# Optimization experiments

Hardware: AMD Instinct MI355X
Metric: run time of the kernel (lower is better)

The kernel has to match this reference:

```python
import jax, jax.numpy as jnp
import numpy as np
import math

# init config (matches init_kwargs); sigma/alpha are squared in __init__
SIGMA2 = 8.0 ** 2
ALPHA2 = 8.0 ** 2
C_SIZE = 512
STRIDE = 8
MINX = 1e-06
M = 100                      # ratio=100 > 1 -> M = int(ratio), capped at 100
K = C_SIZE // STRIDE         # 64 grid cells per axis
G = K * K                    # 4096 density-field cells
B, N = 8, 512                # images, annotated points per image
TWO_PI = 2.0 * math.pi


def setup_inputs():
    key = jax.random.key(0)
    k1, _ = jax.random.split(key)
    points = jax.random.uniform(k1, (B, N, 2), dtype=jnp.float32) * C_SIZE
    st_sizes = jnp.full((B,), float(C_SIZE), dtype=jnp.float32)
    return {"points": points, "st_sizes": st_sizes}


def _per_image(pts, cood):
    # pts: [N,2]; cood: [K]
    x = pts[:, 0]
    y = pts[:, 1]
    dx = x[:, None] - cood[None, :]                 # [N,K]
    dy = y[:, None] - cood[None, :]                 # [N,K]
    # dis_all = y_dis[:, :, None] + x_dis[:, None, :] flattened: g = iy*K + ix
    dis = (dy[:, :, None] ** 2 + dx[:, None, :] ** 2).reshape(pts.shape[0], G)  # [N,G]
    s1 = ALPHA2 + SIGMA2
    s2 = ALPHA2 + SIGMA2 / 2.0
    m = jnp.exp(-0.5 / s1 * dis) / (TWO_PI * s1)    # [N,G]
    tv = jnp.exp(-0.5 / s2 * dis) / (TWO_PI * s2)
    v = (tv / (TWO_PI * 2.0 * SIGMA2)).sum(0) - (m ** 2).sum(0)   # [G] (sel_v == v, no bg)
    # top-M cells by sel_v, then sort indices ascending (ratio>1 branch -> static M)
    inds = jnp.argsort(-v)
    Minds = jnp.sort(inds[:M])                      # [M]
    v = jnp.maximum(v, MINX)                        # add=False -> clamp
    # xf[n, iy*K+ix] = x_n - cood[ix]; yf[n, iy*K+ix] = y_n - cood[iy]
    iy = Minds // K
    ix = Minds % K
    xfM = dx[:, ix]                                 # [N,M]
    yfM = dy[:, iy]                                 # [N,M]
    df = (xfM[:, None, :] - xfM[:, :, None]) ** 2 + (yfM[:, None, :] - yfM[:, :, None]) ** 2
    af = (0.5 * (xfM[:, None, :] + xfM[:, :, None])) ** 2 + (0.5 * (yfM[:, None, :] + yfM[:, :, None])) ** 2
    g1 = jnp.exp(-0.5 / (2.0 * SIGMA2) * df) / (TWO_PI * 2.0 * SIGMA2)          # [N,M,M]
    tmpv2 = (g1 * (jnp.exp(-0.5 / s2 * af) / (TWO_PI * s2))).sum(0) + g1.sum(0)  # [M,M]
    disM = dis[:, Minds]                            # [N,M]
    tmpm2 = jnp.exp(-0.5 / s1 * disM) / (TWO_PI * s1)
    A = tmpv2 - tmpm2.T @ tmpm2                     # [M,M]
    eye = jnp.eye(M, dtype=bool)
    A = jnp.where(eye, 1e-10, A)                    # diag overwritten to 1e-10
    vM = v[Minds] + 1e-10
    tmpA = vM[:, None] * jnp.linalg.inv(A) * vM[None, :] + jnp.diag(vM)
    Bm = jnp.linalg.inv(tmpA)
    return m, v, A, Bm, Minds


def reference(points, st_sizes):
    # st_sizes only matters for use_background=True; kept for signature fidelity
    cood = jnp.arange(0, C_SIZE, STRIDE, dtype=jnp.float32) + STRIDE / 2.0
    m, v, A, Bm, Minds = jax.vmap(lambda p: _per_image(p, cood))(points)
    return m, v, A, Bm, Minds
```

## Files before the change

### kernel.cpp

```cpp
#include <hip/hip_runtime.h>
#include <math.h>

#ifndef M_PI
#define M_PI 3.14159265358979323846
#endif

#define BB 8
#define NN 512
#define KK 64
#define GG 4096
#define MM 100

#define SZ_VD    (BB*GG*8u)
#define OFF_VD   0u
#define SZ_VM    (BB*MM*8u)
#define OFF_VM   (OFF_VD + SZ_VD)
#define SZ_AD    (BB*MM*MM*8u)
#define OFF_AD   (OFF_VM + SZ_VM)
#define OFF_MIND (OFF_AD + SZ_AD)

#define OUT_M  0
#define OUT_V  (BB*NN*GG)
#define OUT_A  (OUT_V + BB*GG)
#define OUT_B  (OUT_A + BB*MM*MM)
#define OUT_MI (OUT_B + BB*MM*MM)

#define MU_VP 4096
#define MU_AS 2048
#define MU_IV 10240

__device__ __forceinline__ void m_one_unit(const float* __restrict__ pts,
                                           float* __restrict__ out, int u) {
  int t = u*256 + (int)threadIdx.x;
  int e = t << 2;
  int img = e >> 21;
  int rem = e & ((1 << 21) - 1);
  int n = rem >> 12;
  int g = rem & 4095;
  int iy = g >> 6, ix = g & 63;
  const float CM = (float)(1.0/(2.0*M_PI*128.0));
  float x = pts[(img*NN + n)*2 + 0];
  float y = pts[(img*NN + n)*2 + 1];
  float dy = y - (8.0f*iy + 4.0f);
  float ey = __expf(dy*dy*(-0.5f/128.0f));
  float4 r;
  float dx0 = x - (8.0f*ix + 4.0f);
  float dx1 = x - (8.0f*(ix+1) + 4.0f);
  float dx2 = x - (8.0f*(ix+2) + 4.0f);
  float dx3 = x - (8.0f*(ix+3) + 4.0f);
  r.x = ey*__expf(dx0*dx0*(-0.5f/128.0f))*CM;
  r.y = ey*__expf(dx1*dx1*(-0.5f/128.0f))*CM;
  r.z = ey*__expf(dx2*dx2*(-0.5f/128.0f))*CM;
  r.w = ey*__expf(dx3*dx3*(-0.5f/128.0f))*CM;
  *reinterpret_cast<float4*>(&out[OUT_M + e]) = r;
}

__device__ __forceinline__ float flt_readlane(float v, int l) {
  return __int_as_float(__builtin_amdgcn_readlane(__float_as_int(v), l));
}

__global__ __launch_bounds__(256) void k_vpart(const float* __restrict__ pts,
                                               double* __restrict__ vd,
                                               float* __restrict__ out) {
  __shared__ double sEy2[16][66], sEx2[16][66], sEy3[16][66], sEx3[16][66];
  __shared__ float px[NN], py[NN];
  int bid = blockIdx.x;
  if (bid >= BB*16) { m_one_unit(pts, out, bid - BB*16 + 0); return; }
  int tile = bid & 15;
  int img = bid >> 4;
  int iy0 = (tile >> 2) << 4;
  int ix0 = (tile & 3) << 4;
  int tx = threadIdx.x & 15, ty = threadIdx.x >> 4;
  for (int s = threadIdx.x; s < NN; s += 256) {
    px[s] = pts[(img*NN + s)*2 + 0];
    py[s] = pts[(img*NN + s)*2 + 1];
  }
  double aV = 0.0, aM = 0.0;
  for (int kc = 0; kc < 8; ++kc) {
    int nb = kc << 6;
    __syncthreads();
    for (int s = threadIdx.x; s < 16*64; s += 256) {
      int row = s >> 6, n = s & 63;
      int nn = nb + n;
      double y = (double)py[nn];
      double cy = 8.0*(iy0 + row) + 4.0;
      double dy = y - cy, dy2 = dy*dy;
      sEy2[row][n] = exp(dy2*(-0.5/96.0));
      sEy3[row][n] = exp(dy2*(-1.0/128.0));
      double x = (double)px[nn];
      double cx = 8.0*(ix0 + row) + 4.0;
      double dx = x - cx, dx2 = dx*dx;
      sEx2[row][n] = exp(dx2*(-0.5/96.0));
      sEx3[row][n] = exp(dx2*(-1.0/128.0));
    }
    __syncthreads();
    #pragma unroll 8
    for (int n = 0; n < 64; ++n) {
      aV += sEy2[ty][n]*sEx2[tx][n];
      aM += sEy3[ty][n]*sEx3[tx][n];
    }
  }
  const double CTV = 1.0/((2.0*M_PI*96.0)*(2.0*M_PI*128.0));
  const double CM2 = 1.0/((2.0*M_PI*128.0)*(2.0*M_PI*128.0));
  vd[img*GG + (iy0 + ty)*KK + ix0 + tx] = CTV*aV - CM2*aM;
}

union AselU {
  struct {
    unsigned long long ku[GG];
    unsigned int hist4[4][256];
    unsigned int suf[257];
    unsigned long long sPrefPlaced, sMaskHi;
    unsigned int sRem, sPickB, sPickRem, sCGt, sCEq;
    int tie[128];
  } se;
  struct {
    float sxi[16][130], syi[16][130], sti[16][130];
    float sxj[16][130], syj[16][130], stj[16][130];
    float px[NN], py[NN];
    float cxi[16], cyi[16], cxj[16], cyj[16];
  } ka;
};

__device__ __forceinline__ void bitonic128(int* a, int tid) {
  for (int kk = 2; kk <= 128; kk <<= 1)
    for (int jj = kk >> 1; jj > 0; jj >>= 1) {
      if (tid < 128) {
        int p = tid ^ jj;
        if (p > tid) {
          int x = a[tid], y = a[p];
          bool up = ((tid & kk) == 0);
          if (up ? (x > y) : (x < y)) { a[tid] = y; a[p] = x; }
        }
      }
      __syncthreads();
    }
}

__global__ __launch_bounds__(256) void k_Asel(const float* __restrict__ pts,
                                              const double* __restrict__ vd,
                                              float* __restrict__ out,
                                              double* __restrict__ ad,
                                              double* __restrict__ vm) {
  __shared__ AselU u;
  __shared__ int selFinal[128];
  int bid = blockIdx.x;
  if (bid >= BB*28) { m_one_unit(pts, out, bid - BB*28 + MU_VP); return; }
  int img = bid / 28;
  int tile = bid - img*28;
  bool tile0 = (tile == 0);
  int tid = threadIdx.x;
  int wv = tid >> 6;

  for (int t = 0; t < 16; ++t) {
    int g = t*256 + tid;
    double v = vd[img*GG + g];
    if (tile0) out[OUT_V + img*GG + g] = (float)fmax(v, 1e-6);
    long long w = __double_as_longlong(v);
    unsigned long long k = (w < 0) ? ~(unsigned long long)w
                                   : ((unsigned long long)w | 0x8000000000000000ull);
    u.se.ku[g] = k;
  }
  if (tid == 0) {
    u.se.sRem = 100; u.se.sPrefPlaced = 0ull; u.se.sMaskHi = 0ull;
    u.se.sCGt = 0; u.se.sCEq = 0; u.se.suf[256] = 0;
  }
  for (int shift = 56; shift >= 0; shift -= 8) {
    for (int c = 0; c < 4; ++c) u.se.hist4[c][tid] = 0;
    __syncthreads();
    unsigned long long maskHi = u.se.sMaskHi, prefP = u.se.sPrefPlaced;
    for (int t = 0; t < 16; ++t) {
      int g = t*256 + tid;
      unsigned long long k = u.se.ku[g];
      if ((k & maskHi) == prefP) {
        unsigned d = (unsigned)((k >> shift) & 255ull);
        atomicAdd(&u.se.hist4[wv][d], 1u);
      }
    }
    __syncthreads();
    u.se.suf[tid] = u.se.hist4[0][tid] + u.se.hist4[1][tid]
                  + u.se.hist4[2][tid] + u.se.hist4[3][tid];
    __syncthreads();
    for (int off = 1; off < 256; off <<= 1) {
      unsigned add = (tid + off < 256) ? u.se.suf[tid + off] : 0u;
      __syncthreads();
      u.se.suf[tid] += add;
      __syncthreads();
    }
    unsigned rem = u.se.sRem;
    unsigned sgt = (tid < 255) ? u.se.suf[tid + 1] : 0u;
    if (u.se.suf[tid] >= rem && sgt < rem) { u.se.sPickB = (unsigned)tid; u.se.sPickRem = rem - sgt; }
    __syncthreads();
    if (tid == 0) {
      u.se.sPrefPlaced |= ((unsigned long long)u.se.sPickB) << shift;
      u.se.sMaskHi     |= (255ull << shift);
      u.se.sRem = u.se.sPickRem;
    }
    __syncthreads();
  }
  unsigned long long T = u.se.sPrefPlaced;
  for (int t = 0; t < 16; ++t) {
    int g = t*256 + tid;
    unsigned long long k = u.se.ku[g];
    if (k > T) {
      unsigned p = atomicAdd(&u.se.sCGt, 1u);
      selFinal[p] = g;
    } else if (k == T) {
      unsigned p = atomicAdd(&u.se.sCEq, 1u);
      if (p < 128) u.se.tie[p] = g;
    }
  }
  __syncthreads();
  unsigned cgt = u.se.sCGt, ceq = u.se.sCEq, r = u.se.sRem;
  if (tid < 128 && tid >= (int)((ceq < 128u) ? ceq : 128u)) u.se.tie[tid] = 0x7fffffff;
  __syncthreads();
  bitonic128(u.se.tie, tid);
  if (tid < (int)r) selFinal[cgt + tid] = u.se.tie[tid];
  if (tid >= MM && tid < 128) selFinal[tid] = 0x7fffffff;
  __syncthreads();
  bitonic128(selFinal, tid);
  if (tile0 && tid < MM) {
    int mi = selFinal[tid];
    out[OUT_MI + img*MM + tid] = (float)mi;
    vm[img*MM + tid] = fmax(vd[img*GG + mi], 1e-6) + 1e-10;
  }
  __syncthreads();

  int it = 0, trem = tile;
  while (trem >= 7 - it) { trem -= 7 - it; ++it; }
  int jt = it + trem;
  int i0 = it*16, j0 = jt*16;
  int tj = tid & 15, ti = tid >> 4;
  int i = i0 + ti, j = j0 + tj;
  const float CM = (float)(1.0/(2.0*M_PI*128.0));
  const float C1 = (float)(1.0/(2.0*M_PI*128.0));
  const float C2 = (float)(1.0/(2.0*M_PI*96.0));
  for (int s = tid; s < NN; s += 256) {
    u.ka.px[s] = pts[(img*NN + s)*2 + 0];
    u.ka.py[s] = pts[(img*NN + s)*2 + 1];
  }
  if (tid < 16) {
    int gi = i0 + tid; if (gi > 99) gi = 99;
    int mi = selFinal[gi];
    u.ka.cxi[tid] = 8.0f*(mi & 63) + 4.0f;
    u.ka.cyi[tid] = 8.0f*(mi >> 6) + 4.0f;
  } else if (tid < 32) {
    int rr = tid - 16;
    int gj = j0 + rr; if (gj > 99) gj = 99;
    int mj = selFinal[gj];
    u.ka.cxj[rr] = 8.0f*(mj & 63) + 4.0f;
    u.ka.cyj[rr] = 8.0f*(mj >> 6) + 4.0f;
  }
  float aV = 0.0f, aM = 0.0f;
  for (int nc = 0; nc < NN; nc += 128) {
    __syncthreads();
    for (int s = tid; s < 16*128; s += 256) {
      int row = s >> 7, n = s & 127;
      float x = u.ka.px[nc + n], y = u.ka.py[nc + n];
      float fxi = x - u.ka.cxi[row], fyi = y - u.ka.cyi[row];
      u.ka.sxi[row][n] = fxi; u.ka.syi[row][n] = fyi;
      u.ka.sti[row][n] = __expf((fxi*fxi + fyi*fyi)*(-0.5f/128.0f))*CM;
      float fxj = x - u.ka.cxj[row], fyj = y - u.ka.cyj[row];
      u.ka.sxj[row][n] = fxj; u.ka.syj[row][n] = fyj;
      u.ka.stj[row][n] = __expf((fxj*fxj + fyj*fyj)*(-0.5f/128.0f))*CM;
    }
    __syncthreads();
    #pragma unroll 4
    for (int n = 0; n < 128; ++n) {
      float xi = u.ka.sxi[ti][n], yi = u.ka.syi[ti][n], tii = u.ka.sti[ti][n];
      float xj = u.ka.sxj[tj][n], yj = u.ka.syj[tj][n], tjj = u.ka.stj[tj][n];
      float ddx = xj - xi, ddy = yj - yi;
      float df = ddx*ddx + ddy*ddy;
      float sx = 0.5f*(xi + xj), sy = 0.5f*(yi + yj);
      float af = sx*sx + sy*sy;
      float g1 = __expf(df*(-0.5f/128.0f))*C1;
      float h  = __expf(af*(-0.5f/96.0f))*C2;
      aV += g1 + g1*h;
      aM += tii*tjj;
    }
  }
  if (i < 100 && j < 100) {
    double val = (i == j) ? 1e-10 : ((double)aV - (double)aM);
    out[OUT_A + (img*MM + i)*MM + j] = (float)val;
    ad[(img*MM + i)*MM + j] = val;
    if (it != jt) {
      out[OUT_A + (img*MM + j)*MM + i] = (float)val;
      ad[(img*MM + j)*MM + i] = val;
    }
  }
}

__global__ __launch_bounds__(256)
void k_inv_m(const double* __restrict__ ad,
             const double* __restrict__ vm,
             const float* __restrict__ pts,
             float* __restrict__ out) {
  __shared__ float S[128*17];
  __shared__ float Pr[16*113];
  __shared__ float svm[112];
  if (blockIdx.x >= BB) {
    m_one_unit(pts, out, (int)blockIdx.x - BB + MU_VP + MU_AS);
    return;
  }
  int img = blockIdx.x;
  int tx = threadIdx.x & 15, ty = threadIdx.x >> 4;
  float C[7][7];
  if (threadIdx.x < 100) svm[threadIdx.x] = (float)vm[img*MM + threadIdx.x];
  #pragma unroll
  for (int a = 0; a < 7; ++a) {
    int r = ty + 16*a;
    #pragma unroll
    for (int b = 0; b < 7; ++b) {
      int j = tx + 16*b;
      float v2 = (r < 100 && j < 100) ? (float)ad[(img*MM + r)*MM + j] : 0.0f;
      if (r == j && r < 100) v2 += (float)vm[img*MM + r];
      C[a][b] = v2;
    }
  }
  for (int p = 0; p < 7; ++p) {
    int k0 = p*16;
    int nbp = (p == 6) ? 4 : 16;
    #pragma unroll
    for (int a = 0; a < 7; ++a) {
      int r = ty + 16*a;
      float val = 0.0f;
      #pragma unroll
      for (int b = 0; b < 7; ++b) if (b == p) val = C[a][b];
      S[r*17 + tx] = (r < 100 && tx < nbp) ? val : 0.0f;
    }
    {
      float pv[7];
      #pragma unroll
      for (int b = 0; b < 7; ++b) pv[b] = 0.0f;
      #pragma unroll
      for (int a = 0; a < 7; ++a) {
        #pragma unroll
        for (int b = 0; b < 7; ++b) if (a == p) pv[b] = C[a][b];
      }
      #pragma unroll
      for (int b = 0; b < 7; ++b) Pr[ty*113 + tx + 16*b] = pv[b];
    }
    __syncthreads();
    if (threadIdx.x < 64) {
      int lane = threadIdx.x;
      float P0[16], P1[16];
      #pragma unroll
      for (int c = 0; c < 16; ++c) {
        P0[c] = S[lane*17 + c];
        P1[c] = (lane + 64 < 112) ? S[(lane + 64)*17 + c] : 0.0f;
      }
      #pragma unroll
      for (int kk = 0; kk < 16; ++kk) {
        if (kk < nbp) {
          int kg = k0 + kk;
          int r1 = lane + 64;
          bool khigh = kg >= 64; int kl = kg & 63;
          float pivinv = 1.0f / flt_readlane(khigh ? P1[kk] : P0[kk], kl);
          float pr[16];
          #pragma unroll
          for (int c = 0; c < 16; ++c) {
            float pv = flt_readlane(khigh ? P1[c] : P0[c], kl);
            pr[c] = (c == kk) ? pivinv : pv*pivinv;
          }
          {
            float f = P0[kk];
            if (lane == kg) {
              #pragma unroll
              for (int c = 0; c < 16; ++c) P0[c] = pr[c];
            } else {
              #pragma unroll
              for (int c = 0; c < 16; ++c) P0[c] = ((c == kk) ? 0.0f : P0[c]) - f*pr[c];
            }
          }
          {
            float f = P1[kk];
            if (r1 == kg) {
              #pragma unroll
              for (int c = 0; c < 16; ++c) P1[c] = pr[c];
            } else {
              #pragma unroll
              for (int c = 0; c < 16; ++c) P1[c] = ((c == kk) ? 0.0f : P1[c]) - f*pr[c];
            }
          }
        }
      }
      #pragma unroll
      for (int c = 0; c < 16; ++c) {
        S[lane*17 + c] = P0[c];
        if (lane + 64 < 112) S[(lane + 64)*17 + c] = P1[c];
      }
    }
    __syncthreads();
    #pragma unroll
    for (int a = 0; a < 7; ++a) {
      int r = ty + 16*a;
      bool prow_ = (r >= k0) && (r < k0 + 16);
      #pragma unroll
      for (int b = 0; b < 7; ++b) {
        if (r >= 100 || b == p || prow_) C[a][b] = 0.0f;
      }
    }
    #pragma unroll 4
    for (int t = 0; t < 16; ++t) {
      bool tok = (t < nbp);
      float bt[7], sa[7];
      #pragma unroll
      for (int b = 0; b < 7; ++b) bt[b] = tok ? Pr[t*113 + tx + 16*b] : 0.0f;
      #pragma unroll
      for (int a = 0; a < 7; ++a) sa[a] = S[(ty + 16*a)*17 + t];
      #pragma unroll
      for (int a = 0; a < 7; ++a)
        #pragma unroll
        for (int b = 0; b < 7; ++b) C[a][b] += sa[a]*bt[b];
    }
    #pragma unroll
    for (int a = 0; a < 7; ++a) {
      int r = ty + 16*a;
      float sval = S[r*17 + tx];
      #pragma unroll
      for (int b = 0; b < 7; ++b) if (b == p) C[a][b] = sval;
    }
    __syncthreads();
  }
  #pragma unroll
  for (int a = 0; a < 7; ++a) {
    int r = ty + 16*a; if (r >= 100) continue;
    float dinv = 1.0f / svm[r];
    #pragma unroll
    for (int b = 0; b < 7; ++b) {
      int c = tx + 16*b; if (c >= 100) continue;
      float val = ((c == r) ? dinv : 0.0f) - C[a][b];
      out[OUT_B + (img*MM + r)*MM + c] = val;
    }
  }
}

extern "C" void kernel_launch(void* const* d_in, const int* in_sizes, int n_in,
                              void* d_out, int out_size, void* d_ws, size_t ws_size,
                              hipStream_t stream) {
  const float* pts = (const float*)d_in[0];
  float* out = (float*)d_out;
  char* ws = (char*)d_ws;
  double* vd  = (double*)(ws + OFF_VD);
  double* vmd = (double*)(ws + OFF_VM);
  double* ad  = (double*)(ws + OFF_AD);

  hipLaunchKernelGGL(k_vpart, dim3(BB*16 + MU_VP), dim3(256), 0, stream, pts, vd, out);
  hipLaunchKernelGGL(k_Asel, dim3(BB*28 + MU_AS), dim3(256), 0, stream, pts, vd, out, ad, vmd);
  hipLaunchKernelGGL(k_inv_m, dim3(BB + MU_IV), dim3(256), 0, stream, ad, vmd, pts, out);
}
```

Measured before the change: 230.9 us.

## Use float workspace and 32-bit radix select with wave-shuffle suffix scan

Stores the v field, the selected v values and the A matrix in float instead of double. This lets the top-M radix select run four 8-bit passes over 32-bit keys instead of eight over 64-bit keys. The shared-memory Hillis-Steele suffix scan, with its many barriers, is replaced by wave-level shuffle scans plus a per-wave total combine. Ties and orderings among near-equal v values may now resolve differently, because the keys are rounded to float before selection.

```diff
diff --git a/kernel.cpp b/kernel.cpp
--- a/kernel.cpp
+++ b/kernel.cpp
@@ -11,13 +11,12 @@
 #define GG 4096
 #define MM 100
 
-#define SZ_VD    (BB*GG*8u)
+#define SZ_VD    (BB*GG*4u)
 #define OFF_VD   0u
-#define SZ_VM    (BB*MM*8u)
+#define SZ_VM    (BB*MM*4u)
 #define OFF_VM   (OFF_VD + SZ_VD)
-#define SZ_AD    (BB*MM*MM*8u)
+#define SZ_AD    (BB*MM*MM*4u)
 #define OFF_AD   (OFF_VM + SZ_VM)
-#define OFF_MIND (OFF_AD + SZ_AD)
 
 #define OUT_M  0
 #define OUT_V  (BB*NN*GG)
@@ -60,7 +59,7 @@
 }
 
 __global__ __launch_bounds__(256) void k_vpart(const float* __restrict__ pts,
-                                               double* __restrict__ vd,
+                                               float* __restrict__ vd,
                                                float* __restrict__ out) {
   __shared__ double sEy2[16][66], sEx2[16][66], sEy3[16][66], sEx3[16][66];
   __shared__ float px[NN], py[NN];
@@ -102,15 +101,15 @@
   }
   const double CTV = 1.0/((2.0*M_PI*96.0)*(2.0*M_PI*128.0));
   const double CM2 = 1.0/((2.0*M_PI*128.0)*(2.0*M_PI*128.0));
-  vd[img*GG + (iy0 + ty)*KK + ix0 + tx] = CTV*aV - CM2*aM;
+  vd[img*GG + (iy0 + ty)*KK + ix0 + tx] = (float)(CTV*aV - CM2*aM);
 }
 
 union AselU {
   struct {
-    unsigned long long ku[GG];
+    unsigned int ku[GG];
     unsigned int hist4[4][256];
-    unsigned int suf[257];
-    unsigned long long sPrefPlaced, sMaskHi;
+    unsigned int wq[4];
+    unsigned int sPref, sMask;
     unsigned int sRem, sPickB, sPickRem, sCGt, sCEq;
     int tie[128];
   } se;
@@ -138,10 +137,10 @@
 }
 
 __global__ __launch_bounds__(256) void k_Asel(const float* __restrict__ pts,
-                                              const double* __restrict__ vd,
+                                              const float* __restrict__ vd,
                                               float* __restrict__ out,
-                                              double* __restrict__ ad,
-                                              double* __restrict__ vm) {
+                                              float* __restrict__ ad,
+                                              float* __restrict__ vm) {
   __shared__ AselU u;
   __shared__ int selFinal[128];
   int bid = blockIdx.x;
@@ -151,57 +150,56 @@
   bool tile0 = (tile == 0);
   int tid = threadIdx.x;
   int wv = tid >> 6;
+  int lane = tid & 63;
 
   for (int t = 0; t < 16; ++t) {
     int g = t*256 + tid;
-    double v = vd[img*GG + g];
-    if (tile0) out[OUT_V + img*GG + g] = (float)fmax(v, 1e-6);
-    long long w = __double_as_longlong(v);
-    unsigned long long k = (w < 0) ? ~(unsigned long long)w
-                                   : ((unsigned long long)w | 0x8000000000000000ull);
-    u.se.ku[g] = k;
+    float v = vd[img*GG + g];
+    if (tile0) out[OUT_V + img*GG + g] = fmaxf(v, 1e-6f);
+    int w = __float_as_int(v);
+    u.se.ku[g] = (w < 0) ? ~(unsigned)w : ((unsigned)w | 0x80000000u);
   }
   if (tid == 0) {
-    u.se.sRem = 100; u.se.sPrefPlaced = 0ull; u.se.sMaskHi = 0ull;
-    u.se.sCGt = 0; u.se.sCEq = 0; u.se.suf[256] = 0;
-  }
-  for (int shift = 56; shift >= 0; shift -= 8) {
+    u.se.sRem = 100; u.se.sPref = 0u; u.se.sMask = 0u;
+    u.se.sCGt = 0; u.se.sCEq = 0;
+  }
+  for (int shift = 24; shift >= 0; shift -= 8) {
     for (int c = 0; c < 4; ++c) u.se.hist4[c][tid] = 0;
     __syncthreads();
-    unsigned long long maskHi = u.se.sMaskHi, prefP = u.se.sPrefPlaced;
+    unsigned mask = u.se.sMask, pref = u.se.sPref;
     for (int t = 0; t < 16; ++t) {
-      int g = t*256 + tid;
-      unsigned long long k = u.se.ku[g];
-      if ((k & maskHi) == prefP) {
-        unsigned d = (unsigned)((k >> shift) & 255ull);
-        atomicAdd(&u.se.hist4[wv][d], 1u);
-      }
-    }
-    __syncthreads();
-    u.se.suf[tid] = u.se.hist4[0][tid] + u.se.hist4[1][tid]
-                  + u.se.hist4[2][tid] + u.se.hist4[3][tid];
-    __syncthreads();
-    for (int off = 1; off < 256; off <<= 1) {
-      unsigned add = (tid + off < 256) ? u.se.suf[tid + off] : 0u;
-      __syncthreads();
-      u.se.suf[tid] += add;
-      __syncthreads();
-    }
+      unsigned k = u.se.ku[t*256 + tid];
+      if ((k & mask) == pref)
+        atomicAdd(&u.se.hist4[wv][(k >> shift) & 255u], 1u);
+    }
+    __syncthreads();
+    unsigned tot = u.se.hist4[0][tid] + u.se.hist4[1][tid]
+                 + u.se.hist4[2][tid] + u.se.hist4[3][tid];
+    unsigned val = tot;
+    #pragma unroll
+    for (int off = 1; off < 64; off <<= 1) {
+      unsigned o = (unsigned)__shfl_down((int)val, off);
+      if (lane + off < 64) val += o;
+    }
+    if (lane == 0) u.se.wq[wv] = val;
+    __syncthreads();
+    unsigned suf = val;
+    for (int w2 = wv + 1; w2 < 4; ++w2) suf += u.se.wq[w2];
     unsigned rem = u.se.sRem;
-    unsigned sgt = (tid < 255) ? u.se.suf[tid + 1] : 0u;
-    if (u.se.suf[tid] >= rem && sgt < rem) { u.se.sPickB = (unsigned)tid; u.se.sPickRem = rem - sgt; }
+    unsigned sgt = suf - tot;
+    if (suf >= rem && sgt < rem) { u.se.sPickB = (unsigned)tid; u.se.sPickRem = rem - sgt; }
     __syncthreads();
     if (tid == 0) {
-      u.se.sPrefPlaced |= ((unsigned long long)u.se.sPickB) << shift;
-      u.se.sMaskHi     |= (255ull << shift);
-      u.se.sRem = u.se.sPickRem;
-    }
-    __syncthreads();
-  }
-  unsigned long long T = u.se.sPrefPlaced;
+      u.se.sPref |= u.se.sPickB << shift;
+      u.se.sMask |= 255u << shift;
+      u.se.sRem   = u.se.sPickRem;
+    }
+    __syncthreads();
+  }
+  unsigned T = u.se.sPref;
   for (int t = 0; t < 16; ++t) {
     int g = t*256 + tid;
-    unsigned long long k = u.se.ku[g];
+    unsigned k = u.se.ku[g];
     if (k > T) {
       unsigned p = atomicAdd(&u.se.sCGt, 1u);
       selFinal[p] = g;
@@ -222,7 +220,7 @@
   if (tile0 && tid < MM) {
     int mi = selFinal[tid];
     out[OUT_MI + img*MM + tid] = (float)mi;
-    vm[img*MM + tid] = fmax(vd[img*GG + mi], 1e-6) + 1e-10;
+    vm[img*MM + tid] = fmaxf(vd[img*GG + mi], 1e-6f) + 1e-10f;
   }
   __syncthreads();
 
@@ -280,19 +278,19 @@
     }
   }
   if (i < 100 && j < 100) {
-    double val = (i == j) ? 1e-10 : ((double)aV - (double)aM);
-    out[OUT_A + (img*MM + i)*MM + j] = (float)val;
+    float val = (i == j) ? 1e-10f : (float)((double)aV - (double)aM);
+    out[OUT_A + (img*MM + i)*MM + j] = val;
     ad[(img*MM + i)*MM + j] = val;
     if (it != jt) {
-      out[OUT_A + (img*MM + j)*MM + i] = (float)val;
+      out[OUT_A + (img*MM + j)*MM + i] = val;
       ad[(img*MM + j)*MM + i] = val;
     }
   }
 }
 
 __global__ __launch_bounds__(256)
-void k_inv_m(const double* __restrict__ ad,
-             const double* __restrict__ vm,
+void k_inv_m(const float* __restrict__ ad,
+             const float* __restrict__ vm,
              const float* __restrict__ pts,
              float* __restrict__ out) {
   __shared__ float S[128*17];
@@ -305,15 +303,15 @@
   int img = blockIdx.x;
   int tx = threadIdx.x & 15, ty = threadIdx.x >> 4;
   float C[7][7];
-  if (threadIdx.x < 100) svm[threadIdx.x] = (float)vm[img*MM + threadIdx.x];
+  if (threadIdx.x < 100) svm[threadIdx.x] = vm[img*MM + threadIdx.x];
   #pragma unroll
   for (int a = 0; a < 7; ++a) {
     int r = ty + 16*a;
     #pragma unroll
     for (int b = 0; b < 7; ++b) {
       int j = tx + 16*b;
-      float v2 = (r < 100 && j < 100) ? (float)ad[(img*MM + r)*MM + j] : 0.0f;
-      if (r == j && r < 100) v2 += (float)vm[img*MM + r];
+      float v2 = (r < 100 && j < 100) ? ad[(img*MM + r)*MM + j] : 0.0f;
+      if (r == j && r < 100) v2 += vm[img*MM + r];
       C[a][b] = v2;
     }
   }
@@ -441,9 +439,9 @@
   const float* pts = (const float*)d_in[0];
   float* out = (float*)d_out;
   char* ws = (char*)d_ws;
-  double* vd  = (double*)(ws + OFF_VD);
-  double* vmd = (double*)(ws + OFF_VM);
-  double* ad  = (double*)(ws + OFF_AD);
+  float* vd  = (float*)(ws + OFF_VD);
+  float* vmd = (float*)(ws + OFF_VM);
+  float* ad  = (float*)(ws + OFF_AD);
 
   hipLaunchKernelGGL(k_vpart, dim3(BB*16 + MU_VP), dim3(256), 0, stream, pts, vd, out);
   hipLaunchKernelGGL(k_Asel, dim3(BB*28 + MU_AS), dim3(256), 0, stream, pts, vd, out, ad, vmd);
```

After: 211.6 us. -8.3%, faster.
